# Optimization experiments

Measured on AMD Instinct MI355X. Metric: run time of the kernel, lower is better.

The kernel has to match this reference:

```python
import jax, jax.numpy as jnp
import numpy as np
from jax import lax

ORDER = 6
WN = 0.5 / 50.0          # highpass_cutoff / (orig_fs/2)
UP, DOWN = 16, 25        # 64/100 reduced by gcd 4 (scipy resample_poly)
HALF_LEN = 10 * DOWN     # scipy kaiser half length = 10*max_rate
NTAPS = 2 * HALF_LEN + 1
PADLEN = 21              # sosfiltfilt default: 3*(2*n_sections+1), 3 biquads
CHANNELS = np.array([126, 125, 48, 112, 67, 93, 10, 61, 39, 108])
D_MODEL = 16
LN_EPS = 1e-5


def _butter_hp_sos(order, wn):
    # scipy.signal.butter(order, wn, btype='high', output='sos') in pure numpy
    fs = 2.0
    warped = 2.0 * fs * np.tan(np.pi * wn / fs)
    m = np.arange(-order + 1, order, 2)
    p = -np.exp(1j * np.pi * m / (2 * order))     # analog LP prototype poles
    k = np.real(1.0 / np.prod(-p))                # lp2hp gain (no zeros)
    p = warped / p                                # lp2hp poles; zeros at s=0
    z = np.zeros(order)
    fs2 = 2.0 * fs                                # bilinear, fs=2
    k = k * np.real(np.prod(fs2 - z) / np.prod(fs2 - p))
    z = (fs2 + z) / (fs2 - z)                     # digital zeros, all +1
    p = (fs2 + p) / (fs2 - p)
    pp = p[np.imag(p) > 0]
    pp = pp[np.argsort(-np.abs(np.abs(pp) - 1.0))]  # closest to unit circle last
    sos = []
    for i, pi in enumerate(pp):
        b = np.array([1.0, -2.0, 1.0]) * (k if i == 0 else 1.0)
        a = np.array([1.0, -2.0 * pi.real, np.abs(pi) ** 2])
        sos.append(np.concatenate([b, a]))
    return np.array(sos)


def _sosfilt_zi(sos):
    # scipy.signal.sosfilt_zi: steady-state of step response per section
    n = sos.shape[0]
    zi = np.zeros((n, 2))
    scale = 1.0
    for s in range(n):
        b0, b1, b2, _, a1, a2 = sos[s]
        A = np.array([[1.0 + a1, -1.0], [a2, 1.0]])
        B = np.array([b1 - a1 * b0, b2 - a2 * b0])
        zi[s] = scale * np.linalg.solve(A, B)
        scale *= (b0 + b1 + b2) / (1.0 + a1 + a2)
    return zi


SOS = _butter_hp_sos(ORDER, WN)
ZI = _sosfilt_zi(SOS)


def _resample_fir():
    # scipy firwin(2*half_len+1, 1/max_rate, window=('kaiser',5.0)) * up
    fc = 1.0 / DOWN
    m = np.arange(NTAPS) - (NTAPS - 1) / 2.0
    h = fc * np.sinc(fc * m) * np.kaiser(NTAPS, 5.0)
    h /= h.sum()
    return h * UP


H_BASE = _resample_fir()


def _pos_encoding(max_len, d):
    pos = np.arange(max_len)[:, None].astype(np.float64)
    div = np.exp(np.arange(0, d, 2) * (-np.log(10000.0) / d))
    pe = np.zeros((max_len, d))
    pe[:, 0::2] = np.sin(pos * div)
    pe[:, 1::2] = np.cos(pos * div)
    return pe.astype(np.float32)


PE = _pos_encoding(3840, D_MODEL)


def _sosfilt(x, zi):
    # x: (N,T), zi: (N,3,2). Cascade of biquads, transposed direct form II.
    sos = jnp.asarray(SOS, x.dtype)
    nsec = SOS.shape[0]

    def step(z, xt):
        v = xt
        zs = []
        for s in range(nsec):  # fixed tiny cascade, unrolled inside scan
            b0, b1, b2, a1, a2 = sos[s, 0], sos[s, 1], sos[s, 2], sos[s, 4], sos[s, 5]
            y = b0 * v + z[s][0]
            zs.append((b1 * v - a1 * y + z[s][1], b2 * v - a2 * y))
            v = y
        return tuple(zs), v

    z0 = tuple((zi[:, s, 0], zi[:, s, 1]) for s in range(nsec))
    _, y = lax.scan(step, z0, x.T)
    return y.T


def _sosfiltfilt(x):
    # scipy.signal.sosfiltfilt with default odd padding, padlen=21
    zi = jnp.asarray(ZI, x.dtype)
    front = 2.0 * x[:, :1] - x[:, PADLEN:0:-1]
    back = 2.0 * x[:, -1:] - x[:, -2:-PADLEN - 2:-1]
    ext = jnp.concatenate([front, x, back], axis=1)
    y = _sosfilt(ext, zi[None] * ext[:, 0, None, None])
    y = y[:, ::-1]
    y = _sosfilt(y, zi[None] * y[:, 0, None, None])
    return y[:, ::-1][:, PADLEN:-PADLEN]


def _resample_poly(x):
    # scipy.signal.resample_poly(x, 64, 100): upfirdn via dilated conv
    T = x.shape[-1]
    n_out = (T * UP) // DOWN + int((T * UP) % DOWN != 0)
    n_pre_pad = DOWN - HALF_LEN % DOWN
    n_pre_remove = (HALF_LEN + n_pre_pad) // DOWN

    def outlen(lh):
        return (((T - 1) * UP + lh) - 1) // DOWN + 1

    n_post = 0
    while outlen(NTAPS + n_pre_pad + n_post) < n_out + n_pre_remove:
        n_post += 1
    h = np.concatenate([np.zeros(n_pre_pad), H_BASE, np.zeros(n_post)])
    L = h.size
    rhs = jnp.asarray(h[::-1].copy(), x.dtype).reshape(1, 1, L)
    y = lax.conv_general_dilated(x[:, None, :], rhs, window_strides=(DOWN,),
                                 padding=[(L - 1, L - 1)], lhs_dilation=(UP,),
                                 dimension_numbers=('NCH', 'OIH', 'NCH'))
    return y[:, 0, n_pre_remove:n_pre_remove + n_out]


def _ln(x, g, b):
    mu = x.mean(-1, keepdims=True)
    var = ((x - mu) ** 2).mean(-1, keepdims=True)
    return (x - mu) * lax.rsqrt(var + LN_EPS) * g + b


def setup_inputs() -> dict:
    key = jax.random.key(0)
    ks = jax.random.split(key, 20)
    f32 = jnp.float32
    d = {
        'x': jax.random.normal(ks[0], (64, 128, 2000), f32),
        'conv_w': jax.random.normal(ks[1], (16, 10, 3), f32) * 0.15,
        'conv_b': jnp.zeros((16,), f32),
        'ln0_g': jnp.ones((16,), f32), 'ln0_b': jnp.zeros((16,), f32),
        'wqkv': jax.random.normal(ks[2], (48, 16), f32) * 0.125,
        'bqkv': jnp.zeros((48,), f32),
        'wo': jax.random.normal(ks[3], (16, 16), f32) * 0.25,
        'bo': jnp.zeros((16,), f32),
        'w1': jax.random.normal(ks[4], (32, 16), f32) * 0.2,
        'b1': jnp.zeros((32,), f32),
        'w2': jax.random.normal(ks[5], (16, 32), f32) * 0.2,
        'b2': jnp.zeros((16,), f32),
        'ln1_g': jnp.ones((16,), f32), 'ln1_b': jnp.zeros((16,), f32),
        'ln2_g': jnp.ones((16,), f32), 'ln2_b': jnp.zeros((16,), f32),
        'wfc': jax.random.normal(ks[6], (1, 16), f32) * 0.3,
        'bfc': jnp.zeros((1,), f32),
    }
    return d


def reference(x, conv_w, conv_b, ln0_g, ln0_b, wqkv, bqkv, wo, bo,
              w1, b1, w2, b2, ln1_g, ln1_b, ln2_g, ln2_b, wfc, bfc):
    B = x.shape[0]
    # remove Cz (last channel) then gather interesting channels
    x = x[:, :-1, :][:, jnp.asarray(CHANNELS), :]        # (B,10,T)
    x = x - x.mean(axis=1, keepdims=True)                # CAR
    C, T = x.shape[1], x.shape[2]
    xf = _sosfiltfilt(x.reshape(B * C, T))               # zero-phase highpass
    xr = _resample_poly(xf)                              # 100 Hz -> 64 Hz
    x = xr.reshape(B, C, -1)
    x = jnp.tanh(x)                                      # artifact_scale = 1.0
    mean = x.mean(axis=2, keepdims=True)                 # zscore, unbiased std
    var = ((x - mean) ** 2).sum(axis=2, keepdims=True) / (x.shape[2] - 1)
    std = jnp.maximum(jnp.sqrt(var), 1e-6)
    x = (x - mean) / std
    # conv1d k=3 pad=1 (10 -> 16) + relu
    x = lax.conv_general_dilated(x, conv_w, (1,), [(1, 1)],
                                 dimension_numbers=('NCH', 'OIH', 'NCH'))
    x = jax.nn.relu(x + conv_b[None, :, None])
    x = x.transpose(0, 2, 1)                             # (B,S,16)
    x = _ln(x, ln0_g, ln0_b)
    x = x + jnp.asarray(PE[:x.shape[1]], x.dtype)[None]
    # TransformerEncoderLayer, post-norm, nhead=1, relu FFN (eval: no dropout)
    qkv = x @ wqkv.T + bqkv
    q, k, v = jnp.split(qkv, 3, axis=-1)
    att = jax.nn.softmax(jnp.einsum('bqd,bkd->bqk', q, k) * 0.25, axis=-1)
    a = jnp.einsum('bqk,bkd->bqd', att, v) @ wo.T + bo
    x = _ln(x + a, ln1_g, ln1_b)
    f = jax.nn.relu(x @ w1.T + b1) @ w2.T + b2
    x = _ln(x + f, ln2_g, ln2_b)
    pooled = x.mean(axis=1)                              # adaptive avg pool -> 1
    return pooled @ wfc.T + bfc                          # (B,1)
```

## Files before the change

### kernel.cpp

```cpp
#include <hip/hip_runtime.h>
#include <cmath>
#include <complex>
#include <algorithm>

#ifndef M_PI
#define M_PI 3.14159265358979323846
#endif

typedef _Float16 f16x8 __attribute__((ext_vector_type(8)));
typedef _Float16 f16x4 __attribute__((ext_vector_type(4)));
typedef __fp16 fp16x2 __attribute__((ext_vector_type(2)));
typedef float f32x4 __attribute__((ext_vector_type(4)));

struct FiltArg {
  double b0[3], b1[3], b2[3], a1[3], a2[3];
  double zi0[3], zi1[3];
};
struct CorArg { double CA[16 * 6]; };
struct EigArg {
  double Pm[36], Pinv[36];
  double czi[6];
  double lam_re[3], lam_im[3];
  double lami_re[3], lami_im[3];
};
struct FirArg { float h[526]; };

static void design_sos(FiltArg& sa) {
  const int order = 6;
  const double wn = 0.5 / 50.0;
  const double fs = 2.0;
  double warped = 2.0 * fs * std::tan(M_PI * wn / fs);
  std::complex<double> p[6];
  for (int i = 0; i < order; i++) {
    int m = -order + 1 + 2 * i;
    p[i] = -std::exp(std::complex<double>(0.0, M_PI * m / (2.0 * order)));
  }
  std::complex<double> prod1(1, 0);
  for (int i = 0; i < 6; i++) prod1 *= -p[i];
  double k = (1.0 / prod1).real();
  for (int i = 0; i < 6; i++) p[i] = warped / p[i];
  const double fs2 = 2.0 * fs;
  std::complex<double> num(1, 0), den(1, 0);
  for (int i = 0; i < 6; i++) { num *= fs2; den *= (fs2 - p[i]); }
  k *= (num / den).real();
  for (int i = 0; i < 6; i++) p[i] = (fs2 + p[i]) / (fs2 - p[i]);
  std::complex<double> pp[3]; int n = 0;
  for (int i = 0; i < 6; i++) if (p[i].imag() > 0) pp[n++] = p[i];
  std::stable_sort(pp, pp + 3,
    [](const std::complex<double>& A, const std::complex<double>& B) {
      return std::fabs(std::abs(A) - 1.0) > std::fabs(std::abs(B) - 1.0);
    });
  double sos[3][6];
  for (int s = 0; s < 3; s++) {
    double g = (s == 0) ? k : 1.0;
    sos[s][0] = g; sos[s][1] = -2.0 * g; sos[s][2] = g;
    sos[s][3] = 1.0; sos[s][4] = -2.0 * pp[s].real(); sos[s][5] = std::norm(pp[s]);
  }
  double scale = 1.0;
  for (int s = 0; s < 3; s++) {
    double b0 = sos[s][0], b1 = sos[s][1], b2 = sos[s][2];
    double a1 = sos[s][4], a2 = sos[s][5];
    double det = 1.0 + a1 + a2;
    double r0 = b1 - a1 * b0, r1 = b2 - a2 * b0;
    double z0 = (r0 + r1) / det;
    double z1 = ((1.0 + a1) * r1 - a2 * r0) / det;
    sa.b0[s] = b0; sa.b1[s] = b1; sa.b2[s] = b2; sa.a1[s] = a1; sa.a2[s] = a2;
    sa.zi0[s] = scale * z0; sa.zi1[s] = scale * z1;
    scale *= (b0 + b1 + b2) / (1.0 + a1 + a2);
  }
}

static double host_step(const FiltArg& c, double z[6], double v) {
  for (int s = 0; s < 3; s++) {
    double y = c.b0[s] * v + z[2 * s];
    z[2 * s]     = c.b1[s] * v - c.a1[s] * y + z[2 * s + 1];
    z[2 * s + 1] = c.b2[s] * v - c.a2[s] * y;
    v = y;
  }
  return v;
}

static void build_filt(FiltArg& c, CorArg& co) {
  design_sos(c);
  for (int j = 0; j < 6; j++) {
    double z[6] = {0, 0, 0, 0, 0, 0};
    z[j] = 1.0;
    for (int i = 0; i < 16; i++) co.CA[i * 6 + j] = host_step(c, z, 0.0);
  }
}

static void build_eig(const FiltArg& c, EigArg& e) {
  double Pr[36];
  for (int s = 0; s < 3; s++) {
    double a1 = c.a1[s], a2 = c.a2[s];
    std::complex<double> disc = std::sqrt(std::complex<double>(a1 * a1 - 4.0 * a2, 0.0));
    std::complex<double> p = (-a1 + disc) / 2.0;
    if (p.imag() < 0) p = std::conj(p);
    std::complex<double> v[6] = {0, 0, 0, 0, 0, 0};
    v[2 * s] = 1.0;
    v[2 * s + 1] = a1 + p;
    std::complex<double> y = 1.0;
    for (int j = s + 1; j < 3; j++) {
      double b0j = c.b0[j], b1j = c.b1[j], b2j = c.b2[j];
      double a1j = c.a1[j], a2j = c.a2[j];
      std::complex<double> det = p * p + a1j * p + a2j;
      std::complex<double> r0 = (b1j - a1j * b0j) * y;
      std::complex<double> r1 = (b2j - a2j * b0j) * y;
      std::complex<double> z0 = (p * r0 + r1) / det;
      std::complex<double> z1 = ((p + a1j) * r1 - a2j * r0) / det;
      v[2 * j] = z0; v[2 * j + 1] = z1;
      y = b0j * y + z0;
    }
    for (int i = 0; i < 6; i++) {
      Pr[i * 6 + 2 * s]     = v[i].real();
      Pr[i * 6 + 2 * s + 1] = v[i].imag();
    }
    std::complex<double> lam = std::pow(p, 16);
    e.lam_re[s] = lam.real(); e.lam_im[s] = lam.imag();
    std::complex<double> li = 1.0 / lam;
    e.lami_re[s] = li.real(); e.lami_im[s] = li.imag();
  }
  for (int i = 0; i < 36; i++) e.Pm[i] = Pr[i];
  double M[6][12];
  for (int i = 0; i < 6; i++)
    for (int j = 0; j < 6; j++) { M[i][j] = Pr[i * 6 + j]; M[i][6 + j] = (i == j) ? 1.0 : 0.0; }
  for (int col = 0; col < 6; col++) {
    int piv = col;
    for (int i = col + 1; i < 6; i++)
      if (std::fabs(M[i][col]) > std::fabs(M[piv][col])) piv = i;
    if (piv != col) for (int j = 0; j < 12; j++) std::swap(M[col][j], M[piv][j]);
    double d = M[col][col];
    for (int j = 0; j < 12; j++) M[col][j] /= d;
    for (int i = 0; i < 6; i++) if (i != col) {
      double f = M[i][col];
      for (int j = 0; j < 12; j++) M[i][j] -= f * M[col][j];
    }
  }
  for (int i = 0; i < 6; i++)
    for (int j = 0; j < 6; j++) e.Pinv[i * 6 + j] = M[i][6 + j];
  double zv[6];
  for (int s = 0; s < 3; s++) { zv[2 * s] = c.zi0[s]; zv[2 * s + 1] = c.zi1[s]; }
  for (int i = 0; i < 6; i++) {
    double sum = 0.0;
    for (int j = 0; j < 6; j++) sum += e.Pinv[i * 6 + j] * zv[j];
    e.czi[i] = sum;
  }
}

static double bessel_i0(double x) {
  double s = 1.0, t = 1.0;
  for (int k = 1; k < 64; k++) {
    double u = x / (2.0 * k);
    t *= u * u; s += t;
    if (t < 1e-18 * s) break;
  }
  return s;
}

static void design_fir(FirArg& fa) {
  double h[501];
  const double fc = 1.0 / 25.0;
  double denom = bessel_i0(5.0);
  double sum = 0.0;
  for (int nn = 0; nn < 501; nn++) {
    double m = nn - 250.0;
    double xx = fc * m;
    double snc = (nn == 250) ? 1.0 : std::sin(M_PI * xx) / (M_PI * xx);
    double r = (2.0 * nn) / 500.0 - 1.0;
    double w = bessel_i0(5.0 * std::sqrt(std::max(0.0, 1.0 - r * r))) / denom;
    h[nn] = fc * snc * w; sum += h[nn];
  }
  for (int nn = 0; nn < 25; nn++) fa.h[nn] = 0.0f;
  for (int nn = 0; nn < 501; nn++) fa.h[25 + nn] = (float)(h[nn] / sum * 16.0);
}

__device__ inline double waveReduceSum(double v) {
  #pragma unroll
  for (int off = 32; off > 0; off >>= 1) v += __shfl_down(v, off, 64);
  return v;
}

__device__ inline void cpow_int(double br, double bi, int n, double& rr_, double& ri_) {
  double rr = 1.0, ri = 0.0;
  while (n) {
    if (n & 1) { double t = rr * br - ri * bi; ri = rr * bi + ri * br; rr = t; }
    double t2 = br * br - bi * bi; bi = 2.0 * br * bi; br = t2;
    n >>= 1;
  }
  rr_ = rr; ri_ = ri;
}

#define XR(t) xr[(t) + ((t) >> 5)]
#define YF(t) yf[(t) + ((t) >> 5)]
__global__ __launch_bounds__(128) void k_filtfilt(const float* __restrict__ xin,
                                                  float* __restrict__ xs,
                                                  float* __restrict__ pe,
                                                  float* __restrict__ out,
                                                  FiltArg c, CorArg co, EigArg eg) {
  int r = blockIdx.x;
  int gk = threadIdx.x;
  if (r >= 640) {
    int i = (r - 640) * 128 + gk;
    int t = i >> 4, d = i & 15, j2 = d >> 1;
    double div = exp(-((double)(2 * j2)) * 0.5756462732485114);
    double a = (double)t * div;
    pe[i] = (float)((d & 1) ? cos(a) : sin(a));
    if (r == 799 && gk < 64) out[gk] = 0.f;
    return;
  }
  __shared__ float xr[2112];
  __shared__ double yf[2112];
  __shared__ double wsum[3][2];
  int lane = gk & 63;
  int wv = gk >> 6;
  int bb = r / 10, cc = r % 10;
  const int ch[10] = {126, 125, 48, 112, 67, 93, 10, 61, 39, 108};
  const float* xb = xin + (size_t)bb * 128 * 2000;
  float* x = xs + (size_t)r * 2000;

  auto xval = [&](int t) -> float {
    float own = 0.f, ssum = 0.f;
    #pragma unroll
    for (int c2 = 0; c2 < 10; c2++) {
      float vv = xb[ch[c2] * 2000 + t];
      ssum += vv;
      if (c2 == cc) own = vv;
    }
    return own - ssum * 0.1f;
  };

  float x0f = xval(0), xlf = xval(1999);
  for (int t = gk; t < 2048; t += 128) {
    float v;
    if (t < 21)        v = 2.f * x0f - xval(21 - t);
    else if (t < 2021) v = xval(t - 21);
    else if (t < 2042) v = 2.f * xlf - xval(4019 - t);
    else               v = 0.f;
    XR(t) = v;
  }
  __syncthreads();

  double b0[3], b1[3], b2[3], a1[3], a2[3];
  #pragma unroll
  for (int s = 0; s < 3; s++) {
    b0[s] = c.b0[s]; b1[s] = c.b1[s]; b2[s] = c.b2[s];
    a1[s] = c.a1[s]; a2[s] = c.a2[s];
  }
  auto step = [&](double* z, double v) -> double {
    #pragma unroll
    for (int s = 0; s < 3; s++) {
      double y = b0[s] * v + z[2 * s];
      z[2 * s]     = b1[s] * v - a1[s] * y + z[2 * s + 1];
      z[2 * s + 1] = b2[s] * v - a2[s] * y;
      v = y;
    }
    return v;
  };

  auto eigscan = [&](double seed, const double* F, double* zst) {
    double G[6];
    #pragma unroll
    for (int i = 0; i < 6; i++) {
      double s = 0.0;
      #pragma unroll
      for (int j = 0; j < 6; j++) s += eg.Pinv[i * 6 + j] * F[j];
      G[i] = s;
    }
    double tre[3], tim[3], sre[3], sim[3];
    #pragma unroll
    for (int s3 = 0; s3 < 3; s3++) {
      double gre = G[2 * s3], gim = -G[2 * s3 + 1];
      double mre, mim;
      cpow_int(eg.lami_re[s3], eg.lami_im[s3], gk, mre, mim);
      tre[s3] = mre * gre - mim * gim;
      tim[s3] = mre * gim + mim * gre;
      double pr = tre[s3], pi = tim[s3];
      #pragma unroll
      for (int off = 1; off < 64; off <<= 1) {
        double ore = __shfl_up(pr, off, 64);
        double oim = __shfl_up(pi, off, 64);
        pr += (lane >= off) ? ore : 0.0;
        pi += (lane >= off) ? oim : 0.0;
      }
      sre[s3] = pr; sim[s3] = pi;
      if (wv == 0 && lane == 63) { wsum[s3][0] = pr; wsum[s3][1] = pi; }
    }
    __syncthreads();
    double coord[6];
    #pragma unroll
    for (int s3 = 0; s3 < 3; s3++) {
      double inc_re = sre[s3] + (wv ? wsum[s3][0] : 0.0);
      double inc_im = sim[s3] + (wv ? wsum[s3][1] : 0.0);
      double Sre = inc_re - tre[s3], Sim = inc_im - tim[s3];
      double c0re = seed * eg.czi[2 * s3];
      double c0im = -seed * eg.czi[2 * s3 + 1];
      double lkre, lkim;
      cpow_int(eg.lam_re[s3], eg.lam_im[s3], gk, lkre, lkim);
      double lm1re = lkre * eg.lami_re[s3] - lkim * eg.lami_im[s3];
      double lm1im = lkre * eg.lami_im[s3] + lkim * eg.lami_re[s3];
      if (gk == 0) { lm1re = 0.0; lm1im = 0.0; }
      double cre = lkre * c0re - lkim * c0im + lm1re * Sre - lm1im * Sim;
      double cim = lkre * c0im + lkim * c0re + lm1re * Sim + lm1im * Sre;
      coord[2 * s3] = cre;
      coord[2 * s3 + 1] = -cim;
    }
    #pragma unroll
    for (int i = 0; i < 6; i++) {
      double s = 0.0;
      #pragma unroll
      for (int j = 0; j < 6; j++) s += eg.Pm[i * 6 + j] * coord[j];
      zst[i] = s;
    }
  };

  int t0 = gk * 16;
  double z[6], yreg[16], zst[6];

  #pragma unroll
  for (int i = 0; i < 6; i++) z[i] = 0.0;
  for (int i = 0; i < 16; i++) yreg[i] = step(z, (double)XR(t0 + i));
  eigscan((double)XR(0), z, zst);
  for (int i = 0; i < 16; i++) {
    double corr = 0.0;
    #pragma unroll
    for (int j = 0; j < 6; j++) corr += co.CA[i * 6 + j] * zst[j];
    YF(t0 + i) = yreg[i] + corr;
  }
  __syncthreads();

  auto rin = [&](int j) -> double { return (j <= 2041) ? YF(2041 - j) : 0.0; };
  double seedB = YF(2041);
  #pragma unroll
  for (int i = 0; i < 6; i++) z[i] = 0.0;
  for (int i = 0; i < 16; i++) yreg[i] = step(z, rin(t0 + i));
  eigscan(seedB, z, zst);
  for (int i = 0; i < 16; i++) {
    int j = t0 + i;
    if (j >= 21 && j <= 2020) {
      double corr = 0.0;
      #pragma unroll
      for (int jj = 0; jj < 6; jj++) corr += co.CA[i * 6 + jj] * zst[jj];
      x[2020 - j] = (float)(yreg[i] + corr);
    }
  }
}

__global__ __launch_bounds__(256) void k_resample_norm(const float* __restrict__ xf,
                                                       float* __restrict__ xn,
                                                       FirArg fa) {
  __shared__ float xl[2000];
  __shared__ float hl[526];
  int r = blockIdx.x;
  const float* x = xf + (size_t)r * 2000;
  for (int i = threadIdx.x; i < 2000; i += 256) xl[i] = x[i];
  for (int i = threadIdx.x; i < 526; i += 256) hl[i] = fa.h[i];
  __syncthreads();
  float vals[5];
  #pragma unroll
  for (int kk = 0; kk < 5; kk++) {
    int o = threadIdx.x + kk * 256;
    int P = 25 * (o + 11);
    int phase = P & 15;
    float acc = 0.f;
    for (int m = phase; m <= 525; m += 16) {
      int idx = (P - m) >> 4;
      if (idx >= 0 && idx < 2000) acc += hl[m] * xl[idx];
    }
    vals[kk] = tanhf(acc);
  }
  double s = 0.0, ss = 0.0;
  #pragma unroll
  for (int kk = 0; kk < 5; kk++) {
    s += (double)vals[kk]; ss += (double)vals[kk] * (double)vals[kk];
  }
  s = waveReduceSum(s); ss = waveReduceSum(ss);
  __shared__ double red[8];
  int wid = threadIdx.x >> 6, lane = threadIdx.x & 63;
  if (lane == 0) { red[wid] = s; red[4 + wid] = ss; }
  __syncthreads();
  double S = red[0] + red[1] + red[2] + red[3];
  double SS = red[4] + red[5] + red[6] + red[7];
  double mean = S / 1280.0;
  double var = (SS - 1280.0 * mean * mean) / 1279.0;
  double sd = fmax(sqrt(fmax(var, 0.0)), 1e-6);
  float fmean = (float)mean, finv = (float)(1.0 / sd);
  #pragma unroll
  for (int kk = 0; kk < 5; kk++)
    xn[(size_t)r * 1280 + threadIdx.x + kk * 256] = (vals[kk] - fmean) * finv;
}

__global__ __launch_bounds__(256) void k_conv_ln_pe_qkv(const float* __restrict__ xn,
    const float* __restrict__ cw, const float* __restrict__ cb,
    const float* __restrict__ g0, const float* __restrict__ bt0,
    const float* __restrict__ wqkv, const float* __restrict__ bqkv,
    const float* __restrict__ pe,
    float* __restrict__ x0, _Float16* __restrict__ Qh,
    _Float16* __restrict__ Kp, _Float16* __restrict__ Vt_g) {
  __shared__ float w[480], bias[16], gg[16], gb[16];
  __shared__ float wq[768], bq[48];
  for (int i = threadIdx.x; i < 480; i += 256) w[i] = cw[i];
  for (int i = threadIdx.x; i < 768; i += 256) wq[i] = wqkv[i];
  if (threadIdx.x < 16) {
    bias[threadIdx.x] = cb[threadIdx.x];
    gg[threadIdx.x] = g0[threadIdx.x];
    gb[threadIdx.x] = bt0[threadIdx.x];
  }
  if (threadIdx.x < 48) bq[threadIdx.x] = bqkv[threadIdx.x];
  __syncthreads();
  int idx = blockIdx.x * 256 + threadIdx.x;
  int b = idx / 1280, t = idx % 1280;
  const float* xb = xn + (size_t)b * 10 * 1280;
  float in[10][3];
  #pragma unroll
  for (int i = 0; i < 10; i++)
    #pragma unroll
    for (int k = 0; k < 3; k++) {
      int tt = t - 1 + k;
      in[i][k] = (tt >= 0 && tt < 1280) ? xb[i * 1280 + tt] : 0.f;
    }
  float o[16];
  #pragma unroll
  for (int oc = 0; oc < 16; oc++) {
    float a = bias[oc];
    #pragma unroll
    for (int i = 0; i < 10; i++)
      #pragma unroll
      for (int k = 0; k < 3; k++) a += in[i][k] * w[oc * 30 + i * 3 + k];
    o[oc] = fmaxf(a, 0.f);
  }
  float mu = 0.f;
  #pragma unroll
  for (int d = 0; d < 16; d++) mu += o[d];
  mu *= (1.f / 16.f);
  float var = 0.f;
  #pragma unroll
  for (int d = 0; d < 16; d++) { float dd = o[d] - mu; var += dd * dd; }
  var *= (1.f / 16.f);
  float inv = 1.f / sqrtf(var + 1e-5f);
  float xv[16];
  float* outp = x0 + (size_t)idx * 16;
  const float* pep = pe + t * 16;
  #pragma unroll
  for (int d = 0; d < 16; d++) {
    xv[d] = (o[d] - mu) * inv * gg[d] + gb[d] + pep[d];
    outp[d] = xv[d];
  }
  _Float16* qh = Qh + (size_t)idx * 16;
  #pragma unroll
  for (int j = 0; j < 16; j++) {
    float a = bq[j];
    #pragma unroll
    for (int d = 0; d < 16; d++) a += xv[d] * wq[j * 16 + d];
    qh[j] = (_Float16)(0.36067376f * a);
  }
  {
    _Float16* kp = Kp + (size_t)idx * 16;
    #pragma unroll
    for (int j = 0; j < 16; j++) {
      float a = bq[16 + j];
      #pragma unroll
      for (int d = 0; d < 16; d++) a += xv[d] * wq[(16 + j) * 16 + d];
      kp[j] = (_Float16)a;
    }
  }
  {
    _Float16* vt = Vt_g + (size_t)b * 16 * 1280 + t;
    #pragma unroll
    for (int j = 0; j < 16; j++) {
      float a = bq[32 + j];
      #pragma unroll
      for (int d = 0; d < 16; d++) a += xv[d] * wq[(32 + j) * 16 + d];
      vt[j * 1280] = (_Float16)a;
    }
  }
}

#define SHIFT2 17.3123404907f
#define KSTR 24
__global__ __launch_bounds__(256) void k_attn_combine(const _Float16* __restrict__ Qh,
    const _Float16* __restrict__ Kp, const _Float16* __restrict__ Vt_g,
    const float* __restrict__ x0,
    const float* __restrict__ wo, const float* __restrict__ bo,
    const float* __restrict__ w1, const float* __restrict__ b1,
    const float* __restrict__ w2, const float* __restrict__ b2,
    const float* __restrict__ g1, const float* __restrict__ bb1,
    const float* __restrict__ g2, const float* __restrict__ bb2,
    const float* __restrict__ wfc, const float* __restrict__ bfc,
    float* __restrict__ out) {
  __shared__ __align__(16) _Float16 Ks[2][128 * KSTR];
  __shared__ __align__(16) _Float16 Vt[2][16 * 136];
  __shared__ float Aly[64][17];
  __shared__ float swo[256], sw1[512], sw2[512];
  __shared__ float sbo[16], sb1[32], sb2[16], sg1[16], sbb1[16], sg2[16], sbb2[16];
  __shared__ float swf[16];
  int tid = threadIdx.x;
  int bid = blockIdx.x;
  int jj  = bid >> 3;
  int b   = (bid & 7) + 8 * (jj & 7);
  int rg  = jj >> 3;
  int wv = tid >> 6;
  int lane = tid & 63;
  int col = lane & 15;
  int quad = lane >> 4;
  size_t base = (size_t)b * 1280;
  int row0 = rg * 64 + wv * 16;

  swo[tid] = wo[tid];
  for (int i = tid; i < 512; i += 256) { sw1[i] = w1[i]; sw2[i] = w2[i]; }
  if (tid < 16) {
    sbo[tid] = bo[tid]; sb2[tid] = b2[tid];
    sg1[tid] = g1[tid]; sbb1[tid] = bb1[tid];
    sg2[tid] = g2[tid]; sbb2[tid] = bb2[tid];
    swf[tid] = wfc[tid];
  }
  if (tid < 32) sb1[tid] = b1[tid];

  f16x8 qf;
  #pragma unroll
  for (int j = 0; j < 8; j++) qf[j] = (_Float16)0.f;
  if (quad < 2)
    qf = *(const f16x8*)(Qh + (base + row0 + col) * 16 + quad * 8);

  f16x8 ones;
  #pragma unroll
  for (int j = 0; j < 8; j++) ones[j] = (_Float16)1.f;
  const f32x4 sfc = {-SHIFT2, -SHIFT2, -SHIFT2, -SHIFT2};

  const _Float16* kp_b = Kp + base * 16;
  const _Float16* vt_b = Vt_g + (size_t)b * 16 * 1280;

  int srow = tid >> 1, shalf = tid & 1;
  int sd = tid >> 4, sseg = tid & 15;

  {
    f16x8 kreg = *(const f16x8*)(kp_b + (size_t)srow * 16 + shalf * 8);
    f16x8 vreg = *(const f16x8*)(vt_b + (size_t)sd * 1280 + sseg * 8);
    *(f16x8*)&Ks[0][srow * KSTR + shalf * 8] = kreg;
    *(f16x8*)&Vt[0][sd * 136 + sseg * 8] = vreg;
  }

  f32x4 oacc = {0.f, 0.f, 0.f, 0.f};
  f32x4 lacc = {0.f, 0.f, 0.f, 0.f};

  int sA = col + ((quad & 1) ? 32 : 0);
  int sB = sA + 16;
  bool hi = (quad >= 2);

  union U32H2 { fp16x2 h; unsigned int u; };
  union PFU { unsigned int u[4]; f16x8 v; };

  for (int s = 0; s < 10; s++) {
    int cur = s & 1;
    __syncthreads();
    f16x8 kreg, vreg;
    if (s < 9) {
      kreg = *(const f16x8*)(kp_b + (size_t)((s + 1) * 128 + srow) * 16 + shalf * 8);
      vreg = *(const f16x8*)(vt_b + (size_t)sd * 1280 + (s + 1) * 128 + sseg * 8);
    }
    const _Float16* ks = &Ks[cur][0];
    const _Float16* vt = &Vt[cur][0];

    unsigned int pp[8][2];
    #pragma unroll
    for (int st = 0; st < 8; st++) {
      f16x8 af;
      #pragma unroll
      for (int j = 0; j < 8; j++) af[j] = (_Float16)0.f;
      if (quad < 2)
        af = *(const f16x8*)&ks[(st * 16 + col) * KSTR + quad * 8];
      f32x4 sf = __builtin_amdgcn_mfma_f32_16x16x32_f16(af, qf, sfc, 0, 0, 0);
      float e0 = __builtin_amdgcn_exp2f(sf[0]);
      float e1 = __builtin_amdgcn_exp2f(sf[1]);
      float e2 = __builtin_amdgcn_exp2f(sf[2]);
      float e3 = __builtin_amdgcn_exp2f(sf[3]);
      U32H2 t0, t1;
      t0.h = __builtin_amdgcn_cvt_pkrtz(e0, e1);
      t1.h = __builtin_amdgcn_cvt_pkrtz(e2, e3);
      pp[st][0] = t0.u;
      pp[st][1] = t1.u;
    }

    f16x8 vfr[4];
    #pragma unroll
    for (int c = 0; c < 4; c++)
      vfr[c] = *(const f16x8*)&vt[col * 136 + c * 32 + quad * 8];

    #pragma unroll
    for (int c = 0; c < 4; c++) {
      int a00 = __shfl((int)pp[2 * c][0], sA, 64);
      int a01 = __shfl((int)pp[2 * c][1], sA, 64);
      int a10 = __shfl((int)pp[2 * c + 1][0], sA, 64);
      int a11 = __shfl((int)pp[2 * c + 1][1], sA, 64);
      int b00 = __shfl((int)pp[2 * c][0], sB, 64);
      int b01 = __shfl((int)pp[2 * c][1], sB, 64);
      int b10 = __shfl((int)pp[2 * c + 1][0], sB, 64);
      int b11 = __shfl((int)pp[2 * c + 1][1], sB, 64);
      PFU pu;
      pu.u[0] = (unsigned int)(hi ? a10 : a00);
      pu.u[1] = (unsigned int)(hi ? a11 : a01);
      pu.u[2] = (unsigned int)(hi ? b10 : b00);
      pu.u[3] = (unsigned int)(hi ? b11 : b01);
      f16x8 pf = pu.v;
      oacc = __builtin_amdgcn_mfma_f32_16x16x32_f16(pf, vfr[c], oacc, 0, 0, 0);
      lacc = __builtin_amdgcn_mfma_f32_16x16x32_f16(pf, ones, lacc, 0, 0, 0);
    }
    if (s < 9) {
      *(f16x8*)&Ks[cur ^ 1][srow * KSTR + shalf * 8] = kreg;
      *(f16x8*)&Vt[cur ^ 1][sd * 136 + sseg * 8] = vreg;
    }
  }

  #pragma unroll
  for (int r = 0; r < 4; r++)
    Aly[wv * 16 + quad * 4 + r][col] = oacc[r] / lacc[r];
  __syncthreads();

  if (tid < 64) {
    int grow = rg * 64 + tid;
    size_t goff = (base + grow) * 16;
    float a[16];
    #pragma unroll
    for (int d = 0; d < 16; d++) a[d] = Aly[tid][d];
    float h[16];
    const float* xr = x0 + goff;
    #pragma unroll
    for (int d = 0; d < 16; d++) {
      float o = sbo[d];
      #pragma unroll
      for (int e = 0; e < 16; e++) o += a[e] * swo[d * 16 + e];
      h[d] = xr[d] + o;
    }
    float mu = 0.f;
    #pragma unroll
    for (int d = 0; d < 16; d++) mu += h[d];
    mu *= (1.f / 16.f);
    float var = 0.f;
    #pragma unroll
    for (int d = 0; d < 16; d++) { float dd = h[d] - mu; var += dd * dd; }
    var *= (1.f / 16.f);
    float inv = 1.f / sqrtf(var + 1e-5f);
    float x1[16];
    #pragma unroll
    for (int d = 0; d < 16; d++) x1[d] = (h[d] - mu) * inv * sg1[d] + sbb1[d];
    float t1[32];
    #pragma unroll
    for (int j = 0; j < 32; j++) {
      float u = sb1[j];
      #pragma unroll
      for (int d = 0; d < 16; d++) u += x1[d] * sw1[j * 16 + d];
      t1[j] = fmaxf(u, 0.f);
    }
    float h2[16];
    #pragma unroll
    for (int d = 0; d < 16; d++) {
      float u = sb2[d];
      #pragma unroll
      for (int j = 0; j < 32; j++) u += t1[j] * sw2[d * 32 + j];
      h2[d] = x1[d] + u;
    }
    mu = 0.f;
    #pragma unroll
    for (int d = 0; d < 16; d++) mu += h2[d];
    mu *= (1.f / 16.f);
    var = 0.f;
    #pragma unroll
    for (int d = 0; d < 16; d++) { float dd = h2[d] - mu; var += dd * dd; }
    var *= (1.f / 16.f);
    inv = 1.f / sqrtf(var + 1e-5f);
    float pv = 0.f;
    #pragma unroll
    for (int d = 0; d < 16; d++)
      pv += ((h2[d] - mu) * inv * sg2[d] + sbb2[d]) * swf[d];
    double part = waveReduceSum((double)pv);
    if (tid == 0) {
      float add = (float)(part / 1280.0);
      if (rg == 0) add += bfc[0];
      atomicAdd(&out[b], add);
    }
  }
}

extern "C" void kernel_launch(void* const* d_in, const int* in_sizes, int n_in,
                              void* d_out, int out_size, void* d_ws, size_t ws_size,
                              hipStream_t stream) {
  const float* x    = (const float*)d_in[0];
  const float* cw   = (const float*)d_in[1];
  const float* cb   = (const float*)d_in[2];
  const float* g0   = (const float*)d_in[3];
  const float* bt0  = (const float*)d_in[4];
  const float* wqkv = (const float*)d_in[5];
  const float* bqkv = (const float*)d_in[6];
  const float* wo   = (const float*)d_in[7];
  const float* bo   = (const float*)d_in[8];
  const float* w1   = (const float*)d_in[9];
  const float* b1   = (const float*)d_in[10];
  const float* w2   = (const float*)d_in[11];
  const float* b2   = (const float*)d_in[12];
  const float* g1   = (const float*)d_in[13];
  const float* bb1  = (const float*)d_in[14];
  const float* g2   = (const float*)d_in[15];
  const float* bb2  = (const float*)d_in[16];
  const float* wfc  = (const float*)d_in[17];
  const float* bfc  = (const float*)d_in[18];
  float* out = (float*)d_out;

  float* ws = (float*)d_ws;
  float* xs = ws;
  float* y1 = xs + 1280000;
  float* xn = y1 + 1306880;
  float* x0 = xn + 819200;
  _Float16* Qh   = (_Float16*)(x0 + 1310720);
  _Float16* Kp   = (_Float16*)(x0 + 1310720 + 655360);
  _Float16* Vt_g = (_Float16*)(x0 + 1310720 + 2 * 655360);
  float* pe = x0 + 1310720 + 3 * 655360;

  FiltArg fc; CorArg co; EigArg eg; FirArg fa;
  build_filt(fc, co);
  build_eig(fc, eg);
  design_fir(fa);

  k_filtfilt<<<800, 128, 0, stream>>>(x, xs, pe, out, fc, co, eg);
  k_resample_norm<<<640, 256, 0, stream>>>(xs, xn, fa);
  k_conv_ln_pe_qkv<<<320, 256, 0, stream>>>(xn, cw, cb, g0, bt0, wqkv, bqkv,
                                            pe, x0, Qh, Kp, Vt_g);
  k_attn_combine<<<1280, 256, 0, stream>>>(Qh, Kp, Vt_g, x0, wo, bo, w1, b1,
                                           w2, b2, g1, bb1, g2, bb2, wfc, bfc,
                                           out);
}
```

Measured before the change: 228.6 us.

## Fuse filtfilt and resample-normalize kernels, stage channel data in LDS, tweak attention loop

Merges the filtfilt kernel and the resample/tanh/zscore kernel into one kernel, so the filtered signal stays in shared memory and never round-trips through global memory. It also computes the re-referenced channel input once into LDS, where the old code recomputed the 10-channel gather per access, and remaps block indices so consecutive blocks come from different batches. In attention, it removes the K padding stride, moves the barrier after the prefetch loads, and loads V fragments inside the PV loop. Costs: one fewer kernel launch, but resampling now runs with 128 threads per block instead of 256, and the unpadded K layout may cause LDS bank conflicts.

```diff
diff --git a/kernel.cpp b/kernel.cpp
--- a/kernel.cpp
+++ b/kernel.cpp
@@ -192,33 +192,38 @@
 
 #define XR(t) xr[(t) + ((t) >> 5)]
 #define YF(t) yf[(t) + ((t) >> 5)]
-__global__ __launch_bounds__(128) void k_filtfilt(const float* __restrict__ xin,
-                                                  float* __restrict__ xs,
-                                                  float* __restrict__ pe,
-                                                  float* __restrict__ out,
-                                                  FiltArg c, CorArg co, EigArg eg) {
-  int r = blockIdx.x;
+__global__ __launch_bounds__(128) void k_filt_resamp(const float* __restrict__ xin,
+                                                     float* __restrict__ xn,
+                                                     float* __restrict__ pe,
+                                                     float* __restrict__ out,
+                                                     FiltArg c, CorArg co, EigArg eg,
+                                                     FirArg fa) {
+  int bid = blockIdx.x;
   int gk = threadIdx.x;
-  if (r >= 640) {
-    int i = (r - 640) * 128 + gk;
+  if (bid >= 640) {
+    int i = (bid - 640) * 128 + gk;
     int t = i >> 4, d = i & 15, j2 = d >> 1;
     double div = exp(-((double)(2 * j2)) * 0.5756462732485114);
     double a = (double)t * div;
     pe[i] = (float)((d & 1) ? cos(a) : sin(a));
-    if (r == 799 && gk < 64) out[gk] = 0.f;
+    if (bid == 799 && gk < 64) out[gk] = 0.f;
     return;
   }
+  int r = (bid & 7) * 80 + (bid >> 3);
+  __shared__ float xd[2000];
   __shared__ float xr[2112];
   __shared__ double yf[2112];
   __shared__ double wsum[3][2];
+  __shared__ float hl[526];
+  __shared__ double red[4];
   int lane = gk & 63;
   int wv = gk >> 6;
   int bb = r / 10, cc = r % 10;
   const int ch[10] = {126, 125, 48, 112, 67, 93, 10, 61, 39, 108};
   const float* xb = xin + (size_t)bb * 128 * 2000;
-  float* x = xs + (size_t)r * 2000;
-
-  auto xval = [&](int t) -> float {
+
+  for (int i = gk; i < 526; i += 128) hl[i] = fa.h[i];
+  for (int t = gk; t < 2000; t += 128) {
     float own = 0.f, ssum = 0.f;
     #pragma unroll
     for (int c2 = 0; c2 < 10; c2++) {
@@ -226,15 +231,16 @@
       ssum += vv;
       if (c2 == cc) own = vv;
     }
-    return own - ssum * 0.1f;
-  };
-
-  float x0f = xval(0), xlf = xval(1999);
+    xd[t] = own - ssum * 0.1f;
+  }
+  __syncthreads();
+
+  float x0f = xd[0], xlf = xd[1999];
   for (int t = gk; t < 2048; t += 128) {
     float v;
-    if (t < 21)        v = 2.f * x0f - xval(21 - t);
-    else if (t < 2021) v = xval(t - 21);
-    else if (t < 2042) v = 2.f * xlf - xval(4019 - t);
+    if (t < 21)        v = 2.f * x0f - xd[21 - t];
+    else if (t < 2021) v = xd[t - 21];
+    else if (t < 2042) v = 2.f * xlf - xd[4019 - t];
     else               v = 0.f;
     XR(t) = v;
   }
@@ -340,53 +346,41 @@
       double corr = 0.0;
       #pragma unroll
       for (int jj = 0; jj < 6; jj++) corr += co.CA[i * 6 + jj] * zst[jj];
-      x[2020 - j] = (float)(yreg[i] + corr);
-    }
-  }
-}
-
-__global__ __launch_bounds__(256) void k_resample_norm(const float* __restrict__ xf,
-                                                       float* __restrict__ xn,
-                                                       FirArg fa) {
-  __shared__ float xl[2000];
-  __shared__ float hl[526];
-  int r = blockIdx.x;
-  const float* x = xf + (size_t)r * 2000;
-  for (int i = threadIdx.x; i < 2000; i += 256) xl[i] = x[i];
-  for (int i = threadIdx.x; i < 526; i += 256) hl[i] = fa.h[i];
+      xd[2020 - j] = (float)(yreg[i] + corr);
+    }
+  }
   __syncthreads();
-  float vals[5];
-  #pragma unroll
-  for (int kk = 0; kk < 5; kk++) {
-    int o = threadIdx.x + kk * 256;
+
+  float vals[10];
+  #pragma unroll
+  for (int kk = 0; kk < 10; kk++) {
+    int o = gk + kk * 128;
     int P = 25 * (o + 11);
     int phase = P & 15;
     float acc = 0.f;
     for (int m = phase; m <= 525; m += 16) {
       int idx = (P - m) >> 4;
-      if (idx >= 0 && idx < 2000) acc += hl[m] * xl[idx];
+      if (idx >= 0 && idx < 2000) acc += hl[m] * xd[idx];
     }
     vals[kk] = tanhf(acc);
   }
   double s = 0.0, ss = 0.0;
   #pragma unroll
-  for (int kk = 0; kk < 5; kk++) {
+  for (int kk = 0; kk < 10; kk++) {
     s += (double)vals[kk]; ss += (double)vals[kk] * (double)vals[kk];
   }
   s = waveReduceSum(s); ss = waveReduceSum(ss);
-  __shared__ double red[8];
-  int wid = threadIdx.x >> 6, lane = threadIdx.x & 63;
-  if (lane == 0) { red[wid] = s; red[4 + wid] = ss; }
+  if (lane == 0) { red[wv] = s; red[2 + wv] = ss; }
   __syncthreads();
-  double S = red[0] + red[1] + red[2] + red[3];
-  double SS = red[4] + red[5] + red[6] + red[7];
+  double S = red[0] + red[1];
+  double SS = red[2] + red[3];
   double mean = S / 1280.0;
   double var = (SS - 1280.0 * mean * mean) / 1279.0;
   double sd = fmax(sqrt(fmax(var, 0.0)), 1e-6);
   float fmean = (float)mean, finv = (float)(1.0 / sd);
   #pragma unroll
-  for (int kk = 0; kk < 5; kk++)
-    xn[(size_t)r * 1280 + threadIdx.x + kk * 256] = (vals[kk] - fmean) * finv;
+  for (int kk = 0; kk < 10; kk++)
+    xn[(size_t)r * 1280 + gk + kk * 128] = (vals[kk] - fmean) * finv;
 }
 
 __global__ __launch_bounds__(256) void k_conv_ln_pe_qkv(const float* __restrict__ xn,
@@ -476,7 +470,6 @@
 }
 
 #define SHIFT2 17.3123404907f
-#define KSTR 24
 __global__ __launch_bounds__(256) void k_attn_combine(const _Float16* __restrict__ Qh,
     const _Float16* __restrict__ Kp, const _Float16* __restrict__ Vt_g,
     const float* __restrict__ x0,
@@ -487,7 +480,7 @@
     const float* __restrict__ g2, const float* __restrict__ bb2,
     const float* __restrict__ wfc, const float* __restrict__ bfc,
     float* __restrict__ out) {
-  __shared__ __align__(16) _Float16 Ks[2][128 * KSTR];
+  __shared__ __align__(16) _Float16 Ks[2][128 * 16];
   __shared__ __align__(16) _Float16 Vt[2][16 * 136];
   __shared__ float Aly[64][17];
   __shared__ float swo[256], sw1[512], sw2[512];
@@ -524,7 +517,6 @@
   f16x8 ones;
   #pragma unroll
   for (int j = 0; j < 8; j++) ones[j] = (_Float16)1.f;
-  const f32x4 sfc = {-SHIFT2, -SHIFT2, -SHIFT2, -SHIFT2};
 
   const _Float16* kp_b = Kp + base * 16;
   const _Float16* vt_b = Vt_g + (size_t)b * 16 * 1280;
@@ -535,7 +527,7 @@
   {
     f16x8 kreg = *(const f16x8*)(kp_b + (size_t)srow * 16 + shalf * 8);
     f16x8 vreg = *(const f16x8*)(vt_b + (size_t)sd * 1280 + sseg * 8);
-    *(f16x8*)&Ks[0][srow * KSTR + shalf * 8] = kreg;
+    *(f16x8*)&Ks[0][srow * 16 + shalf * 8] = kreg;
     *(f16x8*)&Vt[0][sd * 136 + sseg * 8] = vreg;
   }
 
@@ -551,12 +543,12 @@
 
   for (int s = 0; s < 10; s++) {
     int cur = s & 1;
-    __syncthreads();
     f16x8 kreg, vreg;
     if (s < 9) {
       kreg = *(const f16x8*)(kp_b + (size_t)((s + 1) * 128 + srow) * 16 + shalf * 8);
       vreg = *(const f16x8*)(vt_b + (size_t)sd * 1280 + (s + 1) * 128 + sseg * 8);
     }
+    __syncthreads();
     const _Float16* ks = &Ks[cur][0];
     const _Float16* vt = &Vt[cur][0];
 
@@ -567,8 +559,9 @@
       #pragma unroll
       for (int j = 0; j < 8; j++) af[j] = (_Float16)0.f;
       if (quad < 2)
-        af = *(const f16x8*)&ks[(st * 16 + col) * KSTR + quad * 8];
-      f32x4 sf = __builtin_amdgcn_mfma_f32_16x16x32_f16(af, qf, sfc, 0, 0, 0);
+        af = *(const f16x8*)&ks[(st * 16 + col) * 16 + quad * 8];
+      f32x4 sf = {-SHIFT2, -SHIFT2, -SHIFT2, -SHIFT2};
+      sf = __builtin_amdgcn_mfma_f32_16x16x32_f16(af, qf, sf, 0, 0, 0);
       float e0 = __builtin_amdgcn_exp2f(sf[0]);
       float e1 = __builtin_amdgcn_exp2f(sf[1]);
       float e2 = __builtin_amdgcn_exp2f(sf[2]);
@@ -579,11 +572,6 @@
       pp[st][0] = t0.u;
       pp[st][1] = t1.u;
     }
-
-    f16x8 vfr[4];
-    #pragma unroll
-    for (int c = 0; c < 4; c++)
-      vfr[c] = *(const f16x8*)&vt[col * 136 + c * 32 + quad * 8];
 
     #pragma unroll
     for (int c = 0; c < 4; c++) {
@@ -601,11 +589,12 @@
       pu.u[2] = (unsigned int)(hi ? b10 : b00);
       pu.u[3] = (unsigned int)(hi ? b11 : b01);
       f16x8 pf = pu.v;
-      oacc = __builtin_amdgcn_mfma_f32_16x16x32_f16(pf, vfr[c], oacc, 0, 0, 0);
+      f16x8 vf = *(const f16x8*)&vt[col * 136 + c * 32 + quad * 8];
+      oacc = __builtin_amdgcn_mfma_f32_16x16x32_f16(pf, vf, oacc, 0, 0, 0);
       lacc = __builtin_amdgcn_mfma_f32_16x16x32_f16(pf, ones, lacc, 0, 0, 0);
     }
     if (s < 9) {
-      *(f16x8*)&Ks[cur ^ 1][srow * KSTR + shalf * 8] = kreg;
+      *(f16x8*)&Ks[cur ^ 1][srow * 16 + shalf * 8] = kreg;
       *(f16x8*)&Vt[cur ^ 1][sd * 136 + sseg * 8] = vreg;
     }
   }
@@ -719,8 +708,7 @@
   build_eig(fc, eg);
   design_fir(fa);
 
-  k_filtfilt<<<800, 128, 0, stream>>>(x, xs, pe, out, fc, co, eg);
-  k_resample_norm<<<640, 256, 0, stream>>>(xs, xn, fa);
+  k_filt_resamp<<<800, 128, 0, stream>>>(x, xn, pe, out, fc, co, eg, fa);
   k_conv_ln_pe_qkv<<<320, 256, 0, stream>>>(xn, cw, cb, g0, bt0, wqkv, bqkv,
                                             pe, x0, Qh, Kp, Vt_g);
   k_attn_combine<<<1280, 256, 0, stream>>>(Qh, Kp, Vt_g, x0, wo, bo, w1, b1,
```

New measurement: 235.8 us. +3.2%, slower.
